# Kernel tuning notes

Measured on AMD Instinct MI355X. Metric: run time of the kernel, lower is better.

The kernel has to match this reference:

```python
import jax, jax.numpy as jnp
import numpy as np

N_NODES = 100000
N_EDGES = 800000
HIDDEN = 128


def setup_inputs() -> dict:
    key = jax.random.key(0)
    ks = jax.random.split(key, 9)
    h_n = jax.random.normal(ks[0], (N_NODES, HIDDEN), dtype=jnp.float32)
    edge_src = jax.random.randint(ks[1], (N_EDGES,), 0, N_NODES, dtype=jnp.int32)
    edge_dst = jax.random.randint(ks[2], (N_EDGES,), 0, N_NODES, dtype=jnp.int32)
    s = 0.05
    W_w = jax.random.normal(ks[3], (HIDDEN, HIDDEN), dtype=jnp.float32) * s
    W_b = jax.random.normal(ks[4], (HIDDEN,), dtype=jnp.float32) * s
    Ws_w = jax.random.normal(ks[5], (HIDDEN, HIDDEN), dtype=jnp.float32) * s
    Ws_b = jax.random.normal(ks[6], (HIDDEN,), dtype=jnp.float32) * s
    Wt_w = jax.random.normal(ks[7], (HIDDEN, HIDDEN), dtype=jnp.float32) * s
    Wt_b = jax.random.normal(ks[8], (HIDDEN,), dtype=jnp.float32) * s
    return {"h_n": h_n, "edge_src": edge_src, "edge_dst": edge_dst,
            "W_w": W_w, "W_b": W_b, "Ws_w": Ws_w, "Ws_b": Ws_b,
            "Wt_w": Wt_w, "Wt_b": Wt_b}


def reference(h_n, edge_src, edge_dst, W_w, W_b, Ws_w, Ws_b, Wt_w, Wt_b):
    # Dense linears (nn.Linear: x @ W.T + b)
    Wh = h_n @ W_w.T + W_b        # [N,H] used for A @ W(h)
    Wsh = h_n @ Ws_w.T + Ws_b     # [N,H] self term
    Wth = h_n @ Wt_w.T + Wt_b     # [N,H] used for A.T @ W_trans(h)
    # A[src,dst] = 1:  (A @ X)[i]   = sum over edges (i,j) of X[j]
    #              (A.T @ X)[j] = sum over edges (i,j) of X[i]
    agg_fwd = jax.ops.segment_sum(Wh[edge_dst], edge_src, num_segments=N_NODES)
    agg_bwd = jax.ops.segment_sum(Wth[edge_src], edge_dst, num_segments=N_NODES)
    return jax.nn.relu(agg_fwd + Wsh + agg_bwd)
```

## Files before the change

kernel.cpp:

```cpp
#include <hip/hip_runtime.h>
#include <hip/hip_bf16.h>

#define NN 100000
#define NE 800000
#define HIDDEN 128
#define NED (2 * NE)
#define BKN 64
#define NBF 1563
#define NBUCK NBF
#define PS 7
#define CHUNK 4096
#define PBLK ((NED + CHUNK - 1) / CHUNK)

typedef __attribute__((ext_vector_type(8))) short bf16x8;
typedef __attribute__((ext_vector_type(4))) short bf16x4;
typedef __attribute__((ext_vector_type(4))) float f32x4;

__device__ __forceinline__ short f2bf(float f) {
  union { float f; unsigned u; } x; x.f = f;
  unsigned r = x.u + 0x7fffu + ((x.u >> 16) & 1u);
  return (short)(r >> 16);
}
__device__ __forceinline__ float bf2f(short s) {
  union { unsigned u; float f; } x;
  x.u = ((unsigned)(unsigned short)s) << 16;
  return x.f;
}

__global__ __launch_bounds__(256) void convert_weights(
    const float* __restrict__ m0, const float* __restrict__ m1,
    const float* __restrict__ m2, short* __restrict__ out) {
  int i = blockIdx.x * 256 + threadIdx.x;
  int m = i >> 14, j = i & 16383;
  const float* s = (m == 0) ? m0 : (m == 1) ? m1 : m2;
  out[i] = f2bf(s[j]);
}

__global__ __launch_bounds__(256) void convert_h(
    const float* __restrict__ h, short* __restrict__ h_bf) {
  int i = blockIdx.x * 256 + threadIdx.x;
  f32x4 v = *(const f32x4*)(h + (size_t)i * 4);
  bf16x4 o;
#pragma unroll
  for (int j = 0; j < 4; j++) o[j] = f2bf(v[j]);
  *(bf16x4*)(h_bf + (size_t)i * 4) = o;
}

__global__ __launch_bounds__(256) void part_count(
    const int* __restrict__ esrc, const int* __restrict__ edst,
    int* __restrict__ ghist) {
  __shared__ int lh[NBUCK];
  int tid = threadIdx.x;
  for (int i = tid; i < NBUCK; i += 256) lh[i] = 0;
  __syncthreads();
  int base = blockIdx.x * CHUNK;
  int nit = min(CHUNK, NED - base);
  for (int k = tid; k < nit; k += 256) {
    int ed = base + k;
    int b = (ed < NE) ? (esrc[ed] >> 6) : (edst[ed - NE] >> 6);
    atomicAdd(&lh[b], 1);
  }
  __syncthreads();
  for (int i = tid; i < NBUCK; i += 256) {
    int c = lh[i];
    if (c) atomicAdd(ghist + i, c);
  }
}

__global__ __launch_bounds__(1024) void bucket_scan(
    const int* __restrict__ ghist, int* __restrict__ bstart,
    int* __restrict__ gcur) {
  __shared__ int wsum[16];
  __shared__ int woff[16];
  int tid = threadIdx.x;
  int lane = tid & 63, wv = tid >> 6;
  int base = tid * 4;
  int v0 = (base + 0 < NBUCK) ? ghist[base + 0] : 0;
  int v1 = (base + 1 < NBUCK) ? ghist[base + 1] : 0;
  int v2 = (base + 2 < NBUCK) ? ghist[base + 2] : 0;
  int v3 = (base + 3 < NBUCK) ? ghist[base + 3] : 0;
  int s = v0 + v1 + v2 + v3;
  int inc = s;
#pragma unroll
  for (int d = 1; d < 64; d <<= 1) {
    int t = __shfl_up(inc, d, 64);
    if (lane >= d) inc += t;
  }
  if (lane == 63) wsum[wv] = inc;
  __syncthreads();
  if (wv == 0) {
    int x = (lane < 16) ? wsum[lane] : 0;
    int i2 = x;
#pragma unroll
    for (int d = 1; d < 16; d <<= 1) {
      int t = __shfl_up(i2, d, 64);
      if (lane >= d) i2 += t;
    }
    if (lane < 16) woff[lane] = i2 - x;
  }
  __syncthreads();
  int e = woff[wv] + inc - s;
  if (base + 0 < NBUCK) { bstart[base + 0] = e; gcur[base + 0] = e; }
  e += v0;
  if (base + 1 < NBUCK) { bstart[base + 1] = e; gcur[base + 1] = e; }
  e += v1;
  if (base + 2 < NBUCK) { bstart[base + 2] = e; gcur[base + 2] = e; }
  e += v2;
  if (base + 3 < NBUCK) { bstart[base + 3] = e; gcur[base + 3] = e; }
  e += v3;
  if (tid == 1023) bstart[NBUCK] = e;
}

__global__ __launch_bounds__(256) void part_scatter(
    const int* __restrict__ esrc, const int* __restrict__ edst,
    int* __restrict__ gcur, unsigned* __restrict__ ELP) {
  __shared__ int lcur[NBUCK];
  __shared__ int loff[NBUCK];
  __shared__ int gbase[NBUCK];
  __shared__ int psum[256];
  __shared__ unsigned buf[CHUNK];
  __shared__ unsigned short bidA[CHUNK];
  int tid = threadIdx.x;
  for (int i = tid; i < NBUCK; i += 256) lcur[i] = 0;
  __syncthreads();
  int base = blockIdx.x * CHUNK;
  int nit = min(CHUNK, NED - base);
  for (int k = tid; k < nit; k += 256) {
    int ed = base + k;
    int b = (ed < NE) ? (esrc[ed] >> 6) : (edst[ed - NE] >> 6);
    atomicAdd(&lcur[b], 1);
  }
  __syncthreads();
  int s = 0;
  int lo0 = tid * PS, hi0 = min(NBUCK, tid * PS + PS);
  for (int j = lo0; j < hi0; j++) s += lcur[j];
  psum[tid] = s;
  __syncthreads();
  for (int off = 1; off < 256; off <<= 1) {
    int x = psum[tid];
    int add = (tid >= off) ? psum[tid - off] : 0;
    __syncthreads();
    psum[tid] = x + add;
    __syncthreads();
  }
  int run = psum[tid] - s;
  for (int j = lo0; j < hi0; j++) { loff[j] = run; run += lcur[j]; }
  __syncthreads();
  for (int b = tid; b < NBUCK; b += 256) {
    int c = lcur[b];
    if (c) gbase[b] = atomicAdd(gcur + b, c);
    lcur[b] = loff[b];
  }
  __syncthreads();
  for (int k = tid; k < nit; k += 256) {
    int ed = base + k;
    int b, tl, nbr, dir;
    if (ed < NE) { int tg = esrc[ed]; nbr = edst[ed]; b = tg >> 6; tl = tg & 63; dir = 0; }
    else { int e = ed - NE; int tg = edst[e]; nbr = esrc[e]; b = tg >> 6; tl = tg & 63; dir = 1; }
    int slot = atomicAdd(&lcur[b], 1);
    buf[slot] = ((unsigned)dir << 23) | ((unsigned)tl << 17) | (unsigned)nbr;
    bidA[slot] = (unsigned short)b;
  }
  __syncthreads();
  for (int i = tid; i < nit; i += 256) {
    int b = bidA[i];
    ELP[gbase[b] + (i - loff[b])] = buf[i];
  }
}

#define ACC8(V) { a0f+=bf2f((V)[0]); a1f+=bf2f((V)[1]); a2f+=bf2f((V)[2]); a3f+=bf2f((V)[3]); \
                  a4f+=bf2f((V)[4]); a5f+=bf2f((V)[5]); a6f+=bf2f((V)[6]); a7f+=bf2f((V)[7]); }
#define MACC8(M,V) { a0f=fmaf(M,bf2f((V)[0]),a0f); a1f=fmaf(M,bf2f((V)[1]),a1f); \
                     a2f=fmaf(M,bf2f((V)[2]),a2f); a3f=fmaf(M,bf2f((V)[3]),a3f); \
                     a4f=fmaf(M,bf2f((V)[4]),a4f); a5f=fmaf(M,bf2f((V)[5]),a5f); \
                     a6f=fmaf(M,bf2f((V)[6]),a6f); a7f=fmaf(M,bf2f((V)[7]),a7f); }
__global__ __launch_bounds__(512, 4) void fused_gather_gemm(
    const short* __restrict__ h_bf, const unsigned* __restrict__ ELP,
    const int* __restrict__ bstart, const short* __restrict__ Wbf,
    const float* __restrict__ Wb, const float* __restrict__ Wsb,
    const float* __restrict__ Wtb, float* __restrict__ out) {
  __shared__ int sorted[2048];
  __shared__ int cnt[128];
  __shared__ int pfx[128];
  __shared__ int cur[128];
  __shared__ short At[3 * 64 * 136];
  int tid = threadIdx.x;
  int blk = blockIdx.x;
  int node0 = blk * BKN;
  int s = bstart[blk], e = bstart[blk + 1], n = e - s;
  if (tid < 128) cnt[tid] = 0;
  __syncthreads();
  for (int k = tid; k < n; k += 512) atomicAdd(&cnt[ELP[s + k] >> 17], 1);
  for (int p = tid; p < 1024; p += 512) {
    int row = p >> 4, colc = p & 15;
    int nd = node0 + row;
    bf16x8 hv = {0, 0, 0, 0, 0, 0, 0, 0};
    if (nd < NN) hv = *(const bf16x8*)(h_bf + (size_t)nd * HIDDEN + colc * 8);
    *(bf16x8*)(At + row * 136 + colc * 8) = hv;
  }
  __syncthreads();
  int v = (tid < 128) ? cnt[tid] : 0;
  if (tid < 128) pfx[tid] = v;
  __syncthreads();
  for (int off = 1; off < 128; off <<= 1) {
    int add = (tid < 128 && tid >= off) ? pfx[tid - off] : 0;
    __syncthreads();
    if (tid < 128) pfx[tid] += add;
    __syncthreads();
  }
  if (tid < 128) cur[tid] = pfx[tid] - cnt[tid];
  __syncthreads();
  for (int k = tid; k < n; k += 512) {
    unsigned pv = ELP[s + k];
    int slot = atomicAdd(&cur[pv >> 17], 1);
    sorted[slot] = (int)(pv & 0x1FFFFu);
  }
  __syncthreads();
  int qw = tid >> 4, q = tid & 15;
  const short* hb = h_bf + (size_t)q * 8;
#pragma unroll
  for (int t = 0; t < 4; t++) {
    int nd = qw * 4 + t;
    int b0 = pfx[nd];
    int deg = cnt[nd];
    int a0 = b0 - deg;
    float a0f = 0.f, a1f = 0.f, a2f = 0.f, a3f = 0.f;
    float a4f = 0.f, a5f = 0.f, a6f = 0.f, a7f = 0.f;
    if (deg > 0) {
      int lastp = b0 - 1;
      int i0 = sorted[a0];
      int i1 = sorted[min(a0 + 1, lastp)];
      int i2 = sorted[min(a0 + 2, lastp)];
      int i3 = sorted[min(a0 + 3, lastp)];
      bf16x8 v0 = *(const bf16x8*)(hb + (size_t)i0 * HIDDEN);
      bf16x8 v1 = *(const bf16x8*)(hb + (size_t)i1 * HIDDEN);
      bf16x8 v2 = *(const bf16x8*)(hb + (size_t)i2 * HIDDEN);
      bf16x8 v3 = *(const bf16x8*)(hb + (size_t)i3 * HIDDEN);
      int j = a0;
      int ni0 = sorted[min(j + 4, lastp)];
      int ni1 = sorted[min(j + 5, lastp)];
      int ni2 = sorted[min(j + 6, lastp)];
      int ni3 = sorted[min(j + 7, lastp)];
      while (j + 4 <= b0) {
        ACC8(v0); v0 = *(const bf16x8*)(hb + (size_t)ni0 * HIDDEN);
        ACC8(v1); v1 = *(const bf16x8*)(hb + (size_t)ni1 * HIDDEN);
        ACC8(v2); v2 = *(const bf16x8*)(hb + (size_t)ni2 * HIDDEN);
        ACC8(v3); v3 = *(const bf16x8*)(hb + (size_t)ni3 * HIDDEN);
        j += 4;
        ni0 = sorted[min(j + 4, lastp)];
        ni1 = sorted[min(j + 5, lastp)];
        ni2 = sorted[min(j + 6, lastp)];
        ni3 = sorted[min(j + 7, lastp)];
      }
      int r = b0 - j;
      float m1 = (r > 0) ? 1.f : 0.f;
      float m2 = (r > 1) ? 1.f : 0.f;
      float m3 = (r > 2) ? 1.f : 0.f;
      MACC8(m1, v0); MACC8(m2, v1); MACC8(m3, v2);
    }
    short* dst = At + (1 + (nd >> 6)) * 8704 + (nd & 63) * 136 + q * 8;
    bf16x8 o;
    o[0] = f2bf(a0f); o[1] = f2bf(a1f); o[2] = f2bf(a2f); o[3] = f2bf(a3f);
    o[4] = f2bf(a4f); o[5] = f2bf(a5f); o[6] = f2bf(a6f); o[7] = f2bf(a7f);
    *(bf16x8*)dst = o;
  }
  __syncthreads();
  int lane = tid & 63;
  int m16 = lane & 15;
  int kq  = lane >> 4;
  int col0 = (tid >> 6) * 16;
  bf16x8 wf[3][4];
#pragma unroll
  for (int i = 0; i < 3; i++)
#pragma unroll
    for (int t = 0; t < 4; t++)
      wf[i][t] = *(const bf16x8*)(Wbf + i * 16384 + (col0 + m16) * 128 + t * 32 + kq * 8);
  f32x4 bW = *(const f32x4*)(Wb  + col0 + kq * 4);
  f32x4 bS = *(const f32x4*)(Wsb + col0 + kq * 4);
  f32x4 bT = *(const f32x4*)(Wtb + col0 + kq * 4);
#pragma unroll
  for (int g = 0; g < 4; g++) {
    f32x4 acc = {0.f, 0.f, 0.f, 0.f};
    const short* lb = At + (g * 16 + m16) * 136 + kq * 8;
#pragma unroll
    for (int i = 0; i < 3; i++)
#pragma unroll
      for (int t = 0; t < 4; t++) {
        bf16x8 af = *(const bf16x8*)(lb + i * 8704 + t * 32);
        acc = __builtin_amdgcn_mfma_f32_16x16x32_bf16(wf[i][t], af, acc, 0, 0, 0);
      }
    int rl = g * 16 + m16;
    int r = node0 + rl;
    if (r < NN) {
      float dF = (float)cnt[rl];
      float dB = (float)cnt[64 + rl];
      f32x4 vv;
#pragma unroll
      for (int j = 0; j < 4; j++)
        vv[j] = fmaxf(acc[j] + bS[j] + dF * bW[j] + dB * bT[j], 0.f);
      *(f32x4*)(out + (size_t)r * HIDDEN + col0 + kq * 4) = vv;
    }
  }
}

extern "C" void kernel_launch(void* const* d_in, const int* in_sizes, int n_in,
                              void* d_out, int out_size, void* d_ws, size_t ws_size,
                              hipStream_t stream) {
  const float* h    = (const float*)d_in[0];
  const int*   esrc = (const int*)d_in[1];
  const int*   edst = (const int*)d_in[2];
  const float* Ww   = (const float*)d_in[3];
  const float* Wb   = (const float*)d_in[4];
  const float* Wsw  = (const float*)d_in[5];
  const float* Wsb  = (const float*)d_in[6];
  const float* Wtw  = (const float*)d_in[7];
  const float* Wtb  = (const float*)d_in[8];
  float* out = (float*)d_out;

  char* ws = (char*)d_ws;
  int*      ghist  = (int*)(ws + 0);
  int*      bstart = (int*)(ws + 6272);
  int*      gcur   = (int*)(ws + 12544);
  unsigned* ELP    = (unsigned*)(ws + 18816);
  short*    Wbf    = (short*)(ws + 6418816);
  short*    h_bf   = (short*)(ws + 6517120);

  hipMemsetAsync(ghist, 0, NBUCK * sizeof(int), stream);

  convert_weights<<<192, 256, 0, stream>>>(Wsw, Ww, Wtw, Wbf);
  convert_h<<<12500, 256, 0, stream>>>(h, h_bf);
  part_count<<<PBLK, 256, 0, stream>>>(esrc, edst, ghist);
  bucket_scan<<<1, 1024, 0, stream>>>(ghist, bstart, gcur);
  part_scatter<<<PBLK, 256, 0, stream>>>(esrc, edst, gcur, ELP);
  fused_gather_gemm<<<NBF, 512, 0, stream>>>(
      h_bf, ELP, bstart, Wbf, Wb, Wsb, Wtb, out);
}
```

Before: 260.6 us.

## Replace counting-sort edge partition with fixed-capacity bucket atomic scatter

Replaces the count/scan/scatter partitioning pipeline with a single edge_scatter kernel that appends each edge into a fixed-capacity (2048) per-bucket slot using global atomics. The two conversion kernels are merged into one launch. In the fused kernel the self-term rows are read directly from global h_bf instead of being staged in LDS, and the LDS tile uses an XOR swizzle in place of padding. Together with an occupancy hint raised to 6, this cuts LDS use and the number of launches. The cost is contended global atomics and silently dropped edges if a bucket ever exceeds its capacity.

```diff
diff --git a/kernel.cpp b/kernel.cpp
--- a/kernel.cpp
+++ b/kernel.cpp
@@ -7,10 +7,7 @@
 #define NED (2 * NE)
 #define BKN 64
 #define NBF 1563
-#define NBUCK NBF
-#define PS 7
-#define CHUNK 4096
-#define PBLK ((NED + CHUNK - 1) / CHUNK)
+#define BCAP 2048
 
 typedef __attribute__((ext_vector_type(8))) short bf16x8;
 typedef __attribute__((ext_vector_type(4))) short bf16x4;
@@ -27,145 +24,39 @@
   return x.f;
 }
 
-__global__ __launch_bounds__(256) void convert_weights(
-    const float* __restrict__ m0, const float* __restrict__ m1,
-    const float* __restrict__ m2, short* __restrict__ out) {
-  int i = blockIdx.x * 256 + threadIdx.x;
-  int m = i >> 14, j = i & 16383;
-  const float* s = (m == 0) ? m0 : (m == 1) ? m1 : m2;
-  out[i] = f2bf(s[j]);
-}
-
-__global__ __launch_bounds__(256) void convert_h(
-    const float* __restrict__ h, short* __restrict__ h_bf) {
-  int i = blockIdx.x * 256 + threadIdx.x;
-  f32x4 v = *(const f32x4*)(h + (size_t)i * 4);
-  bf16x4 o;
-#pragma unroll
-  for (int j = 0; j < 4; j++) o[j] = f2bf(v[j]);
-  *(bf16x4*)(h_bf + (size_t)i * 4) = o;
-}
-
-__global__ __launch_bounds__(256) void part_count(
-    const int* __restrict__ esrc, const int* __restrict__ edst,
-    int* __restrict__ ghist) {
-  __shared__ int lh[NBUCK];
+__global__ __launch_bounds__(256) void convert_all(
+    const float* __restrict__ h, const float* __restrict__ m0,
+    const float* __restrict__ m1, const float* __restrict__ m2,
+    short* __restrict__ h_bf, short* __restrict__ Wbf) {
+  int blk = blockIdx.x;
   int tid = threadIdx.x;
-  for (int i = tid; i < NBUCK; i += 256) lh[i] = 0;
-  __syncthreads();
-  int base = blockIdx.x * CHUNK;
-  int nit = min(CHUNK, NED - base);
-  for (int k = tid; k < nit; k += 256) {
-    int ed = base + k;
-    int b = (ed < NE) ? (esrc[ed] >> 6) : (edst[ed - NE] >> 6);
-    atomicAdd(&lh[b], 1);
-  }
-  __syncthreads();
-  for (int i = tid; i < NBUCK; i += 256) {
-    int c = lh[i];
-    if (c) atomicAdd(ghist + i, c);
-  }
-}
-
-__global__ __launch_bounds__(1024) void bucket_scan(
-    const int* __restrict__ ghist, int* __restrict__ bstart,
-    int* __restrict__ gcur) {
-  __shared__ int wsum[16];
-  __shared__ int woff[16];
-  int tid = threadIdx.x;
-  int lane = tid & 63, wv = tid >> 6;
-  int base = tid * 4;
-  int v0 = (base + 0 < NBUCK) ? ghist[base + 0] : 0;
-  int v1 = (base + 1 < NBUCK) ? ghist[base + 1] : 0;
-  int v2 = (base + 2 < NBUCK) ? ghist[base + 2] : 0;
-  int v3 = (base + 3 < NBUCK) ? ghist[base + 3] : 0;
-  int s = v0 + v1 + v2 + v3;
-  int inc = s;
-#pragma unroll
-  for (int d = 1; d < 64; d <<= 1) {
-    int t = __shfl_up(inc, d, 64);
-    if (lane >= d) inc += t;
-  }
-  if (lane == 63) wsum[wv] = inc;
-  __syncthreads();
-  if (wv == 0) {
-    int x = (lane < 16) ? wsum[lane] : 0;
-    int i2 = x;
-#pragma unroll
-    for (int d = 1; d < 16; d <<= 1) {
-      int t = __shfl_up(i2, d, 64);
-      if (lane >= d) i2 += t;
-    }
-    if (lane < 16) woff[lane] = i2 - x;
-  }
-  __syncthreads();
-  int e = woff[wv] + inc - s;
-  if (base + 0 < NBUCK) { bstart[base + 0] = e; gcur[base + 0] = e; }
-  e += v0;
-  if (base + 1 < NBUCK) { bstart[base + 1] = e; gcur[base + 1] = e; }
-  e += v1;
-  if (base + 2 < NBUCK) { bstart[base + 2] = e; gcur[base + 2] = e; }
-  e += v2;
-  if (base + 3 < NBUCK) { bstart[base + 3] = e; gcur[base + 3] = e; }
-  e += v3;
-  if (tid == 1023) bstart[NBUCK] = e;
-}
-
-__global__ __launch_bounds__(256) void part_scatter(
+  if (blk < 12500) {
+    int i = blk * 256 + tid;
+    f32x4 v = *(const f32x4*)(h + (size_t)i * 4);
+    bf16x4 o;
+#pragma unroll
+    for (int j = 0; j < 4; j++) o[j] = f2bf(v[j]);
+    *(bf16x4*)(h_bf + (size_t)i * 4) = o;
+  } else {
+    int i = (blk - 12500) * 256 + tid;
+    int m = i >> 14, j = i & 16383;
+    const float* s = (m == 0) ? m0 : (m == 1) ? m1 : m2;
+    Wbf[i] = f2bf(s[j]);
+  }
+}
+
+__global__ __launch_bounds__(256) void edge_scatter(
     const int* __restrict__ esrc, const int* __restrict__ edst,
     int* __restrict__ gcur, unsigned* __restrict__ ELP) {
-  __shared__ int lcur[NBUCK];
-  __shared__ int loff[NBUCK];
-  __shared__ int gbase[NBUCK];
-  __shared__ int psum[256];
-  __shared__ unsigned buf[CHUNK];
-  __shared__ unsigned short bidA[CHUNK];
-  int tid = threadIdx.x;
-  for (int i = tid; i < NBUCK; i += 256) lcur[i] = 0;
-  __syncthreads();
-  int base = blockIdx.x * CHUNK;
-  int nit = min(CHUNK, NED - base);
-  for (int k = tid; k < nit; k += 256) {
-    int ed = base + k;
-    int b = (ed < NE) ? (esrc[ed] >> 6) : (edst[ed - NE] >> 6);
-    atomicAdd(&lcur[b], 1);
-  }
-  __syncthreads();
-  int s = 0;
-  int lo0 = tid * PS, hi0 = min(NBUCK, tid * PS + PS);
-  for (int j = lo0; j < hi0; j++) s += lcur[j];
-  psum[tid] = s;
-  __syncthreads();
-  for (int off = 1; off < 256; off <<= 1) {
-    int x = psum[tid];
-    int add = (tid >= off) ? psum[tid - off] : 0;
-    __syncthreads();
-    psum[tid] = x + add;
-    __syncthreads();
-  }
-  int run = psum[tid] - s;
-  for (int j = lo0; j < hi0; j++) { loff[j] = run; run += lcur[j]; }
-  __syncthreads();
-  for (int b = tid; b < NBUCK; b += 256) {
-    int c = lcur[b];
-    if (c) gbase[b] = atomicAdd(gcur + b, c);
-    lcur[b] = loff[b];
-  }
-  __syncthreads();
-  for (int k = tid; k < nit; k += 256) {
-    int ed = base + k;
-    int b, tl, nbr, dir;
-    if (ed < NE) { int tg = esrc[ed]; nbr = edst[ed]; b = tg >> 6; tl = tg & 63; dir = 0; }
-    else { int e = ed - NE; int tg = edst[e]; nbr = esrc[e]; b = tg >> 6; tl = tg & 63; dir = 1; }
-    int slot = atomicAdd(&lcur[b], 1);
-    buf[slot] = ((unsigned)dir << 23) | ((unsigned)tl << 17) | (unsigned)nbr;
-    bidA[slot] = (unsigned short)b;
-  }
-  __syncthreads();
-  for (int i = tid; i < nit; i += 256) {
-    int b = bidA[i];
-    ELP[gbase[b] + (i - loff[b])] = buf[i];
-  }
+  int i = blockIdx.x * 256 + threadIdx.x;
+  if (i >= NED) return;
+  int b, tl, nbr, dir;
+  if (i < NE) { int tg = esrc[i]; nbr = edst[i]; b = tg >> 6; tl = tg & 63; dir = 0; }
+  else { int e2 = i - NE; int tg = edst[e2]; nbr = esrc[e2]; b = tg >> 6; tl = tg & 63; dir = 1; }
+  int slot = atomicAdd(gcur + b, 1);
+  if (slot < BCAP)
+    ELP[(size_t)b * BCAP + slot] =
+        ((unsigned)dir << 23) | ((unsigned)tl << 17) | (unsigned)nbr;
 }
 
 #define ACC8(V) { a0f+=bf2f((V)[0]); a1f+=bf2f((V)[1]); a2f+=bf2f((V)[2]); a3f+=bf2f((V)[3]); \
@@ -174,30 +65,24 @@
                      a2f=fmaf(M,bf2f((V)[2]),a2f); a3f=fmaf(M,bf2f((V)[3]),a3f); \
                      a4f=fmaf(M,bf2f((V)[4]),a4f); a5f=fmaf(M,bf2f((V)[5]),a5f); \
                      a6f=fmaf(M,bf2f((V)[6]),a6f); a7f=fmaf(M,bf2f((V)[7]),a7f); }
-__global__ __launch_bounds__(512, 4) void fused_gather_gemm(
+__global__ __launch_bounds__(512, 6) void fused_gather_gemm(
     const short* __restrict__ h_bf, const unsigned* __restrict__ ELP,
-    const int* __restrict__ bstart, const short* __restrict__ Wbf,
+    const int* __restrict__ gcur, const short* __restrict__ Wbf,
     const float* __restrict__ Wb, const float* __restrict__ Wsb,
     const float* __restrict__ Wtb, float* __restrict__ out) {
-  __shared__ int sorted[2048];
+  __shared__ int sorted[BCAP];
   __shared__ int cnt[128];
   __shared__ int pfx[128];
   __shared__ int cur[128];
-  __shared__ short At[3 * 64 * 136];
+  __shared__ short At2[2 * 64 * 128];
   int tid = threadIdx.x;
   int blk = blockIdx.x;
   int node0 = blk * BKN;
-  int s = bstart[blk], e = bstart[blk + 1], n = e - s;
+  const unsigned* elp = ELP + (size_t)blk * BCAP;
+  int n = min(gcur[blk], BCAP);
   if (tid < 128) cnt[tid] = 0;
   __syncthreads();
-  for (int k = tid; k < n; k += 512) atomicAdd(&cnt[ELP[s + k] >> 17], 1);
-  for (int p = tid; p < 1024; p += 512) {
-    int row = p >> 4, colc = p & 15;
-    int nd = node0 + row;
-    bf16x8 hv = {0, 0, 0, 0, 0, 0, 0, 0};
-    if (nd < NN) hv = *(const bf16x8*)(h_bf + (size_t)nd * HIDDEN + colc * 8);
-    *(bf16x8*)(At + row * 136 + colc * 8) = hv;
-  }
+  for (int k = tid; k < n; k += 512) atomicAdd(&cnt[elp[k] >> 17], 1);
   __syncthreads();
   int v = (tid < 128) ? cnt[tid] : 0;
   if (tid < 128) pfx[tid] = v;
@@ -211,7 +96,7 @@
   if (tid < 128) cur[tid] = pfx[tid] - cnt[tid];
   __syncthreads();
   for (int k = tid; k < n; k += 512) {
-    unsigned pv = ELP[s + k];
+    unsigned pv = elp[k];
     int slot = atomicAdd(&cur[pv >> 17], 1);
     sorted[slot] = (int)(pv & 0x1FFFFu);
   }
@@ -258,7 +143,7 @@
       float m3 = (r > 2) ? 1.f : 0.f;
       MACC8(m1, v0); MACC8(m2, v1); MACC8(m3, v2);
     }
-    short* dst = At + (1 + (nd >> 6)) * 8704 + (nd & 63) * 136 + q * 8;
+    short* dst = At2 + (nd >> 6) * 8192 + (nd & 63) * 128 + ((q ^ (nd & 7)) * 8);
     bf16x8 o;
     o[0] = f2bf(a0f); o[1] = f2bf(a1f); o[2] = f2bf(a2f); o[3] = f2bf(a3f);
     o[4] = f2bf(a4f); o[5] = f2bf(a5f); o[6] = f2bf(a6f); o[7] = f2bf(a7f);
@@ -269,6 +154,7 @@
   int m16 = lane & 15;
   int kq  = lane >> 4;
   int col0 = (tid >> 6) * 16;
+  int key = m16 & 7;
   bf16x8 wf[3][4];
 #pragma unroll
   for (int i = 0; i < 3; i++)
@@ -281,15 +167,23 @@
 #pragma unroll
   for (int g = 0; g < 4; g++) {
     f32x4 acc = {0.f, 0.f, 0.f, 0.f};
-    const short* lb = At + (g * 16 + m16) * 136 + kq * 8;
-#pragma unroll
-    for (int i = 0; i < 3; i++)
+    int rl = g * 16 + m16;
+    int hr = min(node0 + rl, NN - 1);
+    const short* hrow = h_bf + (size_t)hr * HIDDEN;
+    const short* arow = At2 + rl * 128;
+#pragma unroll
+    for (int t = 0; t < 4; t++) {
+      bf16x8 a0v = *(const bf16x8*)(hrow + kq * 8 + t * 32);
+      acc = __builtin_amdgcn_mfma_f32_16x16x32_bf16(wf[0][t], a0v, acc, 0, 0, 0);
+    }
+#pragma unroll
+    for (int i = 1; i < 3; i++)
 #pragma unroll
       for (int t = 0; t < 4; t++) {
-        bf16x8 af = *(const bf16x8*)(lb + i * 8704 + t * 32);
+        int pc = (kq + 4 * t) ^ key;
+        bf16x8 af = *(const bf16x8*)(arow + (i - 1) * 8192 + pc * 8);
         acc = __builtin_amdgcn_mfma_f32_16x16x32_bf16(wf[i][t], af, acc, 0, 0, 0);
       }
-    int rl = g * 16 + m16;
     int r = node0 + rl;
     if (r < NN) {
       float dF = (float)cnt[rl];
@@ -318,20 +212,15 @@
   float* out = (float*)d_out;
 
   char* ws = (char*)d_ws;
-  int*      ghist  = (int*)(ws + 0);
-  int*      bstart = (int*)(ws + 6272);
-  int*      gcur   = (int*)(ws + 12544);
-  unsigned* ELP    = (unsigned*)(ws + 18816);
-  short*    Wbf    = (short*)(ws + 6418816);
-  short*    h_bf   = (short*)(ws + 6517120);
-
-  hipMemsetAsync(ghist, 0, NBUCK * sizeof(int), stream);
-
-  convert_weights<<<192, 256, 0, stream>>>(Wsw, Ww, Wtw, Wbf);
-  convert_h<<<12500, 256, 0, stream>>>(h, h_bf);
-  part_count<<<PBLK, 256, 0, stream>>>(esrc, edst, ghist);
-  bucket_scan<<<1, 1024, 0, stream>>>(ghist, bstart, gcur);
-  part_scatter<<<PBLK, 256, 0, stream>>>(esrc, edst, gcur, ELP);
+  int*      gcur = (int*)(ws + 0);
+  unsigned* ELP  = (unsigned*)(ws + 6400);
+  short*    Wbf  = (short*)(ws + 12810496);
+  short*    h_bf = (short*)(ws + 12908800);
+
+  hipMemsetAsync(gcur, 0, NBF * sizeof(int), stream);
+
+  convert_all<<<12692, 256, 0, stream>>>(h, Wsw, Ww, Wtw, h_bf, Wbf);
+  edge_scatter<<<(NED + 255) / 256, 256, 0, stream>>>(esrc, edst, gcur, ELP);
   fused_gather_gemm<<<NBF, 512, 0, stream>>>(
-      h_bf, ELP, bstart, Wbf, Wb, Wsb, Wtb, out);
-}
+      h_bf, ELP, gcur, Wbf, Wb, Wsb, Wtb, out);
+}
```

After: 466.9 us. +79.1%, slower.
